# Kernel tuning notes

Hardware: AMD Instinct MI355X
Metric: run time of the kernel (lower is better)

The kernel has to match this reference:

```python
import jax, jax.numpy as jnp
import numpy as np

D_MODEL = 1024
D_STATE = 128
HEAD_DIM = 64
EXPAND = 2
K = 4  # conv_kernel
N_GROUPS = 1
D_INNER = EXPAND * D_MODEL            # 2048
N_HEADS = D_INNER // HEAD_DIM         # 32
D_PROJ = 2 * D_INNER + 2 * N_GROUPS * D_STATE + N_HEADS  # 4384
EPS = 1e-6


def _rmsnorm(x, w):
    return x * jax.lax.rsqrt(jnp.mean(x * x, axis=-1, keepdims=True) + EPS) * w


def setup_inputs() -> dict:
    key = jax.random.key(0)
    ks = jax.random.split(key, 8)
    B, L = 2, 2048
    x = jax.random.normal(ks[0], (B, L, D_MODEL), jnp.float32)
    norm_w = jnp.ones((D_MODEL,), jnp.float32)
    in_proj_w = jax.random.normal(ks[1], (D_PROJ, D_MODEL), jnp.float32) / np.sqrt(D_MODEL).astype(np.float32)
    conv_w = jax.random.normal(ks[2], (D_INNER, K), jnp.float32) / np.sqrt(K).astype(np.float32)
    conv_b = jnp.zeros((D_INNER,), jnp.float32)
    A_log = jnp.log(jax.random.uniform(ks[3], (N_HEADS,), jnp.float32) * 15.0 + 1.0)
    D = jnp.ones((N_HEADS,), jnp.float32)
    dt_bias = jnp.log(jax.random.uniform(ks[4], (N_HEADS,), jnp.float32) * 0.099 + 0.001)
    out_proj_w = jax.random.normal(ks[5], (D_MODEL, D_INNER), jnp.float32) / np.sqrt(D_INNER).astype(np.float32)
    return dict(x=x, norm_w=norm_w, in_proj_w=in_proj_w, conv_w=conv_w, conv_b=conv_b,
                A_log=A_log, D=D, dt_bias=dt_bias, out_proj_w=out_proj_w)


def reference(x, norm_w, in_proj_w, conv_w, conv_b, A_log, D, dt_bias, out_proj_w):
    batch, L, _ = x.shape
    residual = x
    xn = _rmsnorm(x, norm_w)
    proj = jnp.einsum('bld,pd->blp', xn, in_proj_w)  # (B,L,D_PROJ)

    # split fused projection -> z, x_ssm, B, C, dt_raw
    i = 0
    z = proj[:, :, i:i + D_INNER]; i += D_INNER
    x_ssm = proj[:, :, i:i + D_INNER]; i += D_INNER
    bc = N_GROUPS * D_STATE
    Bm = proj[:, :, i:i + bc].reshape(batch, L, N_GROUPS, D_STATE); i += bc
    Cm = proj[:, :, i:i + bc].reshape(batch, L, N_GROUPS, D_STATE); i += bc
    dt_raw = proj[:, :, i:i + N_HEADS]

    # causal depthwise conv1d (left-pad K-1) + SiLU
    xp = jnp.pad(x_ssm, ((0, 0), (K - 1, 0), (0, 0)))
    x_conv = conv_b
    for k in range(K):
        x_conv = x_conv + xp[:, k:k + L, :] * conv_w[:, k]
    x_conv = jax.nn.silu(x_conv)

    xh = x_conv.reshape(batch, L, N_HEADS, HEAD_DIM)
    dt = jax.nn.softplus(dt_raw + dt_bias)          # (B,L,H)
    dA = jnp.exp(-jnp.exp(A_log) * dt)              # (B,L,H)
    dtx = dt[..., None] * xh                        # (B,L,H,P)

    gidx = jnp.arange(N_HEADS) // (N_HEADS // N_GROUPS)
    Bg = Bm[:, :, gidx, :]                          # (B,L,H,N)
    Cg = Cm[:, :, gidx, :]                          # (B,L,H,N)

    def step(h, inp):
        dA_t, dtx_t, B_t, C_t = inp                 # (B,H), (B,H,P), (B,H,N), (B,H,N)
        h = h * dA_t[:, :, None, None] + dtx_t[..., None] * B_t[:, :, None, :]
        y_t = jnp.einsum('bhpn,bhn->bhp', h, C_t)
        return h, y_t

    h0 = jnp.zeros((batch, N_HEADS, HEAD_DIM, D_STATE), jnp.float32)
    xs = (jnp.swapaxes(dA, 0, 1), jnp.swapaxes(dtx, 0, 1),
          jnp.swapaxes(Bg, 0, 1), jnp.swapaxes(Cg, 0, 1))
    _, ys = jax.lax.scan(step, h0, xs)              # ys: (L,B,H,P)
    y = jnp.swapaxes(ys, 0, 1) + D[None, None, :, None] * xh

    y = y.reshape(batch, L, D_INNER) * jax.nn.silu(z)
    return residual + jnp.einsum('bli,di->bld', y, out_proj_w)
```

## Files before the change

kernel.cpp:

```cpp
#include <hip/hip_runtime.h>
#include <hip/hip_bf16.h>

#define L_SEQ 2048
#define DM 1024
#define DI 2048
#define DS 128
#define NH 32
#define HD 64
#define DPROJ 4384
#define DPAD 4480
#define NBATCH 2
#define NCH 8
#define CH 256
#define B_OFF 4096
#define C_OFF 4224
#define DT_OFF 4352
#define SWZ(row) ((((row) ^ ((row) >> 3)) & 7) << 4)

typedef unsigned short u16;
typedef __attribute__((ext_vector_type(8))) short short8;
typedef __attribute__((ext_vector_type(4))) float f32x4;

#define GLL16(g, l)                                                     \
  __builtin_amdgcn_global_load_lds(                                     \
      (const __attribute__((address_space(1))) unsigned int*)(g),       \
      (__attribute__((address_space(3))) unsigned int*)(l), 16, 0, 0)
#define SBAR __builtin_amdgcn_s_barrier()
#define MEMFENCE asm volatile("" ::: "memory")

__device__ __forceinline__ u16 f2bf(float f) {
  union { float f; unsigned u; } c; c.f = f;
  unsigned u = c.u;
  u += 0x7fffu + ((u >> 16) & 1u);
  return (u16)(u >> 16);
}
__device__ __forceinline__ float bf2f(u16 u) {
  return __uint_as_float((unsigned)u << 16);
}
__device__ __forceinline__ float siluf(float x) {
  return x / (1.0f + expf(-x));
}
__device__ __forceinline__ void store_out(u16* C, size_t o, float v) { C[o] = f2bf(v); }
__device__ __forceinline__ void store_out(float* C, size_t o, float v) { C[o] = v; }

__global__ __launch_bounds__(256) void rmsnorm_kernel(
    const float* __restrict__ x, const float* __restrict__ w,
    u16* __restrict__ xnb) {
  int m = blockIdx.x;
  int t = threadIdx.x;
  const float* row = x + (size_t)m * DM;
  float4 v = *(const float4*)(row + t * 4);
  float ss = v.x * v.x + v.y * v.y + v.z * v.z + v.w * v.w;
#pragma unroll
  for (int o = 32; o > 0; o >>= 1) ss += __shfl_xor(ss, o);
  __shared__ float sred[4];
  if ((t & 63) == 0) sred[t >> 6] = ss;
  __syncthreads();
  ss = sred[0] + sred[1] + sred[2] + sred[3];
  float rs = rsqrtf(ss * (1.0f / DM) + 1e-6f);
  float4 wv = *(const float4*)(w + t * 4);
  ushort4 o;
  o.x = f2bf(v.x * rs * wv.x);
  o.y = f2bf(v.y * rs * wv.y);
  o.z = f2bf(v.z * rs * wv.z);
  o.w = f2bf(v.w * rs * wv.w);
  *(ushort4*)(xnb + (size_t)m * DM + t * 4) = o;
}

__global__ __launch_bounds__(256) void cvt_w1_kernel(
    const float* __restrict__ w, u16* __restrict__ o) {
  int r = blockIdx.x;
  int c = threadIdx.x * 4;
  ushort4 u;
  if (r < DPROJ) {
    float4 v = *(const float4*)(w + (size_t)r * DM + c);
    u.x = f2bf(v.x); u.y = f2bf(v.y); u.z = f2bf(v.z); u.w = f2bf(v.w);
  } else {
    u.x = 0; u.y = 0; u.z = 0; u.w = 0;
  }
  *(ushort4*)(o + (size_t)r * DM + c) = u;
}

__global__ __launch_bounds__(256) void cvt_w2_kernel(
    const float* __restrict__ w, u16* __restrict__ o) {
  size_t i = ((size_t)blockIdx.x * 256 + threadIdx.x) * 8;
  float4 v0 = *(const float4*)(w + i);
  float4 v1 = *(const float4*)(w + i + 4);
  ushort4 a, b;
  a.x = f2bf(v0.x); a.y = f2bf(v0.y); a.z = f2bf(v0.z); a.w = f2bf(v0.w);
  b.x = f2bf(v1.x); b.y = f2bf(v1.y); b.z = f2bf(v1.z); b.w = f2bf(v1.w);
  *(ushort4*)(o + i) = a;
  *(ushort4*)(o + i + 4) = b;
}

template <typename OT, bool RES, bool DTS, int BN>
__global__ __launch_bounds__(256, 4) void gemm_bt(
    const u16* __restrict__ A, const u16* __restrict__ Bw,
    OT* __restrict__ C, const float* __restrict__ resid,
    float* __restrict__ dts, int M, int N, int K, int nbx) {
  constexpr int WN = BN / 2;
  constexpr int NJ = WN / 16;
  __shared__ u16 lA[3][128 * 32];
  __shared__ u16 lB[3][BN * 32];
  const int tid = threadIdx.x;
  const int wv = tid >> 6, lane = tid & 63;
  const int wm = wv >> 1, wn = wv & 1;

  const int nwg = gridDim.x;
  const int cpx = nwg >> 3;
  const int wg = blockIdx.x;
  const int swz = (wg & 7) * cpx + (wg >> 3);
  const int m0 = (swz / nbx) * 128, n0 = (swz % nbx) * BN;

  const int rowS = tid >> 2;
  const int colS = (tid & 3) * 8;
  const u16* gA0 = A + (size_t)(m0 + rowS) * K + colS;
  const u16* gA1 = A + (size_t)(m0 + rowS + 64) * K + colS;
  const u16* gB0 = Bw + (size_t)(n0 + rowS) * K + colS;
  const u16* gB1 = Bw + (size_t)(n0 + rowS + 64) * K + colS;

  auto stage = [&](int kt, int buf) {
    const int ko = kt << 5;
    GLL16(gA0 + ko, &lA[buf][wv * 512]);
    GLL16(gA1 + ko, &lA[buf][2048 + wv * 512]);
    GLL16(gB0 + ko, &lB[buf][wv * 512]);
    if (BN == 128) GLL16(gB1 + ko, &lB[buf][2048 + wv * 512]);
  };

  f32x4 acc[4][NJ] = {};
  const int r = lane & 15;
  const int koff = (lane >> 4) * 8;

  auto compute = [&](int buf) {
    short8 af[4], bfr[NJ];
#pragma unroll
    for (int i = 0; i < 4; ++i)
      af[i] = *(const short8*)&lA[buf][(wm * 64 + i * 16 + r) * 32 + koff];
#pragma unroll
    for (int j = 0; j < NJ; ++j)
      bfr[j] = *(const short8*)&lB[buf][(wn * WN + j * 16 + r) * 32 + koff];
#pragma unroll
    for (int i = 0; i < 4; ++i)
#pragma unroll
      for (int j = 0; j < NJ; ++j)
        acc[i][j] = __builtin_amdgcn_mfma_f32_16x16x32_bf16(
            af[i], bfr[j], acc[i][j], 0, 0, 0);
  };

  const int nk = K >> 5;
  stage(0, 0);
  stage(1, 1);
  int cur = 0;
  for (int kt = 0; kt < nk; ++kt) {
    if (kt + 1 < nk) {
      if (BN == 128) asm volatile("s_waitcnt vmcnt(4)" ::: "memory");
      else           asm volatile("s_waitcnt vmcnt(3)" ::: "memory");
    } else {
      asm volatile("s_waitcnt vmcnt(0)" ::: "memory");
    }
    SBAR;
    MEMFENCE;
    if (kt + 2 < nk) {
      int nb = cur + 2; if (nb >= 3) nb -= 3;
      stage(kt + 2, nb);
    }
    compute(cur);
    ++cur; if (cur == 3) cur = 0;
  }

  const int rbase = m0 + wm * 64 + (lane >> 4) * 4;
  const int cbase = n0 + wn * WN + (lane & 15);
#pragma unroll
  for (int i = 0; i < 4; ++i) {
#pragma unroll
    for (int j = 0; j < NJ; ++j) {
      int row0 = rbase + i * 16;
      int col = cbase + j * 16;
#pragma unroll
      for (int rr = 0; rr < 4; ++rr) {
        size_t o = (size_t)(row0 + rr) * N + col;
        float v = acc[i][j][rr];
        if (RES) v += resid[o];
        store_out(C, o, v);
        if (DTS) {
          if (col >= DT_OFF && col < DT_OFF + NH)
            dts[(size_t)(row0 + rr) * NH + (col - DT_OFF)] = v;
        }
      }
    }
  }
}

__global__ __launch_bounds__(256) void conv_kernel(
    const u16* __restrict__ proj, const float* __restrict__ cw,
    const float* __restrict__ cb, u16* __restrict__ xh) {
  int m = blockIdx.x;
  int l = m & (L_SEQ - 1);
  int c0 = threadIdx.x * 8;
  float4 wv[8];
#pragma unroll
  for (int j = 0; j < 8; ++j) wv[j] = *(const float4*)(cw + (size_t)(c0 + j) * 4);
  float acc[8];
#pragma unroll
  for (int j = 0; j < 8; ++j) acc[j] = cb[c0 + j];
#pragma unroll
  for (int k = 0; k < 4; ++k) {
    int lk = l + k - 3;
    if (lk >= 0) {
      short8 rv8 = *(const short8*)(proj + (size_t)(m + k - 3) * DPAD + DI + c0);
#pragma unroll
      for (int j = 0; j < 8; ++j) {
        float wk = (k == 0) ? wv[j].x : (k == 1) ? wv[j].y : (k == 2) ? wv[j].z : wv[j].w;
        acc[j] = fmaf(bf2f((u16)rv8[j]), wk, acc[j]);
      }
    }
  }
  short8 o;
#pragma unroll
  for (int j = 0; j < 8; ++j) o[j] = (short)f2bf(siluf(acc[j]));
  *(short8*)(xh + (size_t)m * DI + c0) = o;
}

__global__ __launch_bounds__(256) void dtda_kernel(
    const float* __restrict__ dts, const float* __restrict__ dt_bias,
    const float* __restrict__ A_log, float* __restrict__ dAdt) {
  int idx = blockIdx.x * 256 + threadIdx.x;
  int h = idx & 31;
  float raw = dts[idx] + dt_bias[h];
  float dt = fmaxf(raw, 0.0f) + log1pf(expf(-fabsf(raw)));
  float a = -expf(A_log[h]) * dt;
  float2 o; o.x = a; o.y = dt;
  *(float2*)(dAdt + (size_t)idx * 2) = o;
}


__global__ __launch_bounds__(512) void scan_state_mfma(
    const u16* __restrict__ proj, const float* __restrict__ dAdt,
    const u16* __restrict__ xhy, float* __restrict__ S,
    float* __restrict__ P) {
  __shared__ u16 sBT[128 * 64];
  __shared__ u16 sXT[64 * 64];
  __shared__ u16 sXW[64 * 64];
  __shared__ float sDt[64], sCum[64], sWs[64], sLam[64];

  const int bid = blockIdx.x;
  const int ch = bid & 7, hh = (bid >> 3) & 31, b = bid >> 8;
  const int tid = threadIdx.x;
  const int w = tid >> 6, l = tid & 63;
  const int tw = w >> 1, half = w & 1;
  const int klane = (l >> 4) * 16;
  const size_t mchunk = (size_t)(b * L_SEQ + ch * CH);

  f32x4 hAcc[4] = {};
  float ctot = 0.0f;

  auto STAGE = [&](int sc) {
    const size_t m0 = mchunk + (size_t)sc * 64;
    {
      const int tp = tid >> 4;
      const int n0 = (tid & 15) * 8;
      const u16* r0 = proj + (m0 + 2 * tp) * DPAD + B_OFF + n0;
      short8 lo8 = *(const short8*)r0;
      short8 hi8 = *(const short8*)(r0 + DPAD);
#pragma unroll
      for (int q = 0; q < 8; ++q) {
        int n = n0 + q;
        unsigned v = (unsigned)(u16)lo8[q] | ((unsigned)(u16)hi8[q] << 16);
        *(unsigned*)((char*)sBT + ((n * 128 + 4 * tp) ^ SWZ(n))) = v;
      }
    }
    {
      const int sx = tid >> 3;
      const int p0 = (tid & 7) * 8;
      short8 xv8 = *(const short8*)(xhy + (m0 + sx) * DI + hh * 64 + p0);
#pragma unroll
      for (int i = 0; i < 8; ++i) {
        int p = p0 + i;
        *(u16*)((char*)sXT + ((p * 128 + 2 * sx) ^ SWZ(p))) = (u16)xv8[i];
      }
    }
    if (tid < 64) {
      float2 ad = *(const float2*)(dAdt + (m0 + tid) * 64 + hh * 2);
      float a = ad.x, dtv = ad.y;
      sDt[tid] = dtv;
      float val = a;
#pragma unroll
      for (int o = 1; o < 64; o <<= 1) {
        float t2 = __shfl_up(val, o);
        if (tid >= o) val += t2;
      }
      sCum[tid] = val;
      float c63 = __shfl(val, 63);
      sWs[tid] = __expf(c63 - val) * dtv;
      sLam[tid] = __expf(val);
    }
  };

  STAGE(0);
  __syncthreads();

  for (int sc = 0; sc < 4; ++sc) {
    {
      int p = tid >> 3, sg = tid & 7;
      int byteX = (p * 128 + sg * 16) ^ SWZ(p);
      short8 xv = *(short8*)((char*)sXT + byteX);
      short8 outp;
#pragma unroll
      for (int j = 0; j < 8; ++j)
        outp[j] = (short)f2bf(bf2f((u16)xv[j]) * sWs[sg * 8 + j]);
      *(short8*)((char*)sXW + byteX) = outp;
    }
    __syncthreads();

    {
      float lam63 = sLam[63];
      ctot += sCum[63];
#pragma unroll
      for (int j = 0; j < 4; ++j) {
        hAcc[j][0] *= lam63; hAcc[j][1] *= lam63;
        hAcc[j][2] *= lam63; hAcc[j][3] *= lam63;
      }
      int prow = tw * 16 + (l & 15);
      short8 aXW[2];
#pragma unroll
      for (int kk = 0; kk < 2; ++kk)
        aXW[kk] = *(short8*)((char*)sXW + ((prow * 128 + kk * 64 + klane) ^ SWZ(prow)));
#pragma unroll
      for (int j = 0; j < 4; ++j) {
        int nrow = (half * 4 + j) * 16 + (l & 15);
#pragma unroll
        for (int kk = 0; kk < 2; ++kk) {
          short8 bBT = *(short8*)((char*)sBT + ((nrow * 128 + kk * 64 + klane) ^ SWZ(nrow)));
          hAcc[j] = __builtin_amdgcn_mfma_f32_16x16x32_bf16(aXW[kk], bBT, hAcc[j], 0, 0, 0);
        }
      }
    }
    __syncthreads();
    if (sc < 3) STAGE(sc + 1);
    __syncthreads();
  }

  float* Sb = S + (size_t)((b * 32 + hh) * NCH + ch) * 8192;
  const int p0 = tw * 16 + (l >> 4) * 4;
#pragma unroll
  for (int j = 0; j < 4; ++j) {
    int n = (half * 4 + j) * 16 + (l & 15);
#pragma unroll
    for (int r = 0; r < 4; ++r)
      Sb[(p0 + r) * 128 + n] = hAcc[j][r];
  }
  if (tid == 0) P[(b * 32 + hh) * NCH + ch] = __expf(ctot);
}

__global__ __launch_bounds__(256) void combine_kernel(
    float* __restrict__ S, const float* __restrict__ P) {
  int tid = blockIdx.x * 256 + threadIdx.x;
  int bh = tid >> 13, pn = tid & 8191;
  size_t base = (size_t)bh * NCH * 8192 + pn;
  float E = 0.0f;
#pragma unroll
  for (int c = 0; c < NCH; ++c) {
    size_t o = base + (size_t)c * 8192;
    float Sc = S[o];
    S[o] = E;
    E = fmaf(P[bh * NCH + c], E, Sc);
  }
}

__global__ __launch_bounds__(512) void scan_y_mfma(
    const u16* __restrict__ proj, const float* __restrict__ dAdt,
    const u16* __restrict__ xhy, const float* __restrict__ Dv,
    const float* __restrict__ S, u16* __restrict__ yb) {
  __shared__ u16 sC[64 * 128];
  __shared__ u16 sB[64 * 128];
  __shared__ u16 sHb[64 * 128];
  __shared__ u16 sBT[128 * 64];
  __shared__ u16 sXT[64 * 64];
  __shared__ u16 sXW[64 * 64];
  __shared__ u16 sW[64 * 64];
  __shared__ float sDt[64], sCum[64], sWs[64], sLam[64];

  const int bid = blockIdx.x;
  const int ch = bid & 7, hh = (bid >> 3) & 31, b = bid >> 8;
  const int tid = threadIdx.x;
  const int w = tid >> 6, l = tid & 63;
  const int tw = w >> 1, half = w & 1;
  const int klane = (l >> 4) * 16;
  const float Dh = Dv[hh];
  const size_t mchunk = (size_t)(b * L_SEQ + ch * CH);

  f32x4 hAcc[4];
  {
    const float* Sb = S + (size_t)((b * 32 + hh) * NCH + ch) * 8192;
    const int p0 = tw * 16 + (l >> 4) * 4;
#pragma unroll
    for (int j = 0; j < 4; ++j) {
      int n = (half * 4 + j) * 16 + (l & 15);
#pragma unroll
      for (int r = 0; r < 4; ++r)
        hAcc[j][r] = Sb[(p0 + r) * 128 + n];
    }
    int p = tid >> 3, sg = tid & 7;
#pragma unroll
    for (int i = 0; i < 4; ++i) {
      float4 v = *(const float4*)(Sb + p * 128 + sg * 16 + 4 * i);
      ushort4 u;
      u.x = f2bf(v.x); u.y = f2bf(v.y); u.z = f2bf(v.z); u.w = f2bf(v.w);
      *(ushort4*)((char*)sHb + ((p * 256 + (sg * 16 + 4 * i) * 2) ^ SWZ(p))) = u;
    }
  }

  auto STAGE = [&](int sc) {
    const size_t m0 = mchunk + (size_t)sc * 64;
    {
      const int tp = tid >> 4;
      const int n0 = (tid & 15) * 8;
      const u16* r0 = proj + (m0 + 2 * tp) * DPAD;
      short8 b0 = *(const short8*)(r0 + B_OFF + n0);
      short8 b1 = *(const short8*)(r0 + DPAD + B_OFF + n0);
      short8 c0v = *(const short8*)(r0 + C_OFF + n0);
      short8 c1v = *(const short8*)(r0 + DPAD + C_OFF + n0);
      *(short8*)((char*)sB + ((2 * tp * 256 + n0 * 2) ^ SWZ(2 * tp))) = b0;
      *(short8*)((char*)sB + (((2 * tp + 1) * 256 + n0 * 2) ^ SWZ(2 * tp + 1))) = b1;
      *(short8*)((char*)sC + ((2 * tp * 256 + n0 * 2) ^ SWZ(2 * tp))) = c0v;
      *(short8*)((char*)sC + (((2 * tp + 1) * 256 + n0 * 2) ^ SWZ(2 * tp + 1))) = c1v;
#pragma unroll
      for (int q = 0; q < 8; ++q) {
        int n = n0 + q;
        unsigned v = (unsigned)(u16)b0[q] | ((unsigned)(u16)b1[q] << 16);
        *(unsigned*)((char*)sBT + ((n * 128 + 4 * tp) ^ SWZ(n))) = v;
      }
    }
    {
      const int sx = tid >> 3;
      const int p0 = (tid & 7) * 8;
      short8 xv8 = *(const short8*)(xhy + (m0 + sx) * DI + hh * 64 + p0);
#pragma unroll
      for (int i = 0; i < 8; ++i) {
        int p = p0 + i;
        *(u16*)((char*)sXT + ((p * 128 + 2 * sx) ^ SWZ(p))) = (u16)xv8[i];
      }
    }
    if (tid < 64) {
      float2 ad = *(const float2*)(dAdt + (m0 + tid) * 64 + hh * 2);
      float a = ad.x, dtv = ad.y;
      sDt[tid] = dtv;
      float val = a;
#pragma unroll
      for (int o = 1; o < 64; o <<= 1) {
        float t2 = __shfl_up(val, o);
        if (tid >= o) val += t2;
      }
      sCum[tid] = val;
      float c63 = __shfl(val, 63);
      sWs[tid] = __expf(c63 - val) * dtv;
      sLam[tid] = __expf(val);
    }
  };

  STAGE(0);
  __syncthreads();

  for (int sc = 0; sc < 4; ++sc) {
    const size_t m0 = mchunk + (size_t)sc * 64;
    {
      int p = tid >> 3, sg = tid & 7;
      int byteX = (p * 128 + sg * 16) ^ SWZ(p);
      short8 xv = *(short8*)((char*)sXT + byteX);
      short8 outp;
#pragma unroll
      for (int j = 0; j < 8; ++j)
        outp[j] = (short)f2bf(bf2f((u16)xv[j]) * sWs[sg * 8 + j]);
      *(short8*)((char*)sXW + byteX) = outp;
    }
    __syncthreads();

    const int trow = tw * 16 + (l & 15);
    short8 aC[4];
#pragma unroll
    for (int kk = 0; kk < 4; ++kk)
      aC[kk] = *(short8*)((char*)sC + ((trow * 256 + kk * 64 + klane) ^ SWZ(trow)));

    {
      f32x4 g[2] = {};
#pragma unroll
      for (int sv2 = 0; sv2 < 2; ++sv2) {
        int srow = (half * 2 + sv2) * 16 + (l & 15);
#pragma unroll
        for (int kk = 0; kk < 4; ++kk) {
          short8 bB = *(short8*)((char*)sB + ((srow * 256 + kk * 64 + klane) ^ SWZ(srow)));
          g[sv2] = __builtin_amdgcn_mfma_f32_16x16x32_bf16(aC[kk], bB, g[sv2], 0, 0, 0);
        }
      }
#pragma unroll
      for (int sv2 = 0; sv2 < 2; ++sv2) {
        int s = (half * 2 + sv2) * 16 + (l & 15);
        float dts_ = sDt[s], cums = sCum[s];
#pragma unroll
        for (int r = 0; r < 4; ++r) {
          int t = tw * 16 + (l >> 4) * 4 + r;
          float v = (t >= s) ? g[sv2][r] * __expf(sCum[t] - cums) * dts_ : 0.0f;
          *(u16*)((char*)sW + ((t * 128 + 2 * s) ^ SWZ(t))) = f2bf(v);
        }
      }
    }
    __syncthreads();

    f32x4 y1[2] = {}, y2[2] = {};
    float lamv[4], lam63 = sLam[63];
#pragma unroll
    for (int r = 0; r < 4; ++r) lamv[r] = sLam[tw * 16 + (l >> 4) * 4 + r];
    {
      short8 aW[2];
#pragma unroll
      for (int kk = 0; kk < 2; ++kk)
        aW[kk] = *(short8*)((char*)sW + ((trow * 128 + kk * 64 + klane) ^ SWZ(trow)));
#pragma unroll
      for (int pv2 = 0; pv2 < 2; ++pv2) {
        int prow = (half * 2 + pv2) * 16 + (l & 15);
#pragma unroll
        for (int kk = 0; kk < 2; ++kk) {
          short8 bX = *(short8*)((char*)sXT + ((prow * 128 + kk * 64 + klane) ^ SWZ(prow)));
          y1[pv2] = __builtin_amdgcn_mfma_f32_16x16x32_bf16(aW[kk], bX, y1[pv2], 0, 0, 0);
        }
#pragma unroll
        for (int kk = 0; kk < 4; ++kk) {
          short8 bH = *(short8*)((char*)sHb + ((prow * 256 + kk * 64 + klane) ^ SWZ(prow)));
          y2[pv2] = __builtin_amdgcn_mfma_f32_16x16x32_bf16(aC[kk], bH, y2[pv2], 0, 0, 0);
        }
      }
#pragma unroll
      for (int j = 0; j < 4; ++j) {
        hAcc[j][0] *= lam63; hAcc[j][1] *= lam63;
        hAcc[j][2] *= lam63; hAcc[j][3] *= lam63;
      }
      short8 aXW[2];
#pragma unroll
      for (int kk = 0; kk < 2; ++kk)
        aXW[kk] = *(short8*)((char*)sXW + ((trow * 128 + kk * 64 + klane) ^ SWZ(trow)));
#pragma unroll
      for (int j = 0; j < 4; ++j) {
        int nrow = (half * 4 + j) * 16 + (l & 15);
#pragma unroll
        for (int kk = 0; kk < 2; ++kk) {
          short8 bBT = *(short8*)((char*)sBT + ((nrow * 128 + kk * 64 + klane) ^ SWZ(nrow)));
          hAcc[j] = __builtin_amdgcn_mfma_f32_16x16x32_bf16(aXW[kk], bBT, hAcc[j], 0, 0, 0);
        }
      }
    }
    __syncthreads();

    {
#pragma unroll
      for (int j = 0; j < 4; ++j) {
        int n = (half * 4 + j) * 16 + (l & 15);
#pragma unroll
        for (int r = 0; r < 4; ++r) {
          int p = tw * 16 + (l >> 4) * 4 + r;
          *(u16*)((char*)sHb + ((p * 256 + 2 * n) ^ SWZ(p))) = f2bf(hAcc[j][r]);
        }
      }
#pragma unroll
      for (int pv2 = 0; pv2 < 2; ++pv2) {
        int p = (half * 2 + pv2) * 16 + (l & 15);
#pragma unroll
        for (int r = 0; r < 4; ++r) {
          int t = tw * 16 + (l >> 4) * 4 + r;
          int col = hh * 64 + p;
          size_t gy = (m0 + t) * DI + col;
          float xv = bf2f(xhy[gy]);
          float yv = y1[pv2][r] + lamv[r] * y2[pv2][r] + Dh * xv;
          float zv = bf2f(proj[(m0 + t) * DPAD + col]);
          yb[gy] = f2bf(yv * siluf(zv));
        }
      }
      if (sc < 3) STAGE(sc + 1);
    }
    __syncthreads();
  }
}

extern "C" void kernel_launch(void* const* d_in, const int* in_sizes, int n_in,
                              void* d_out, int out_size, void* d_ws, size_t ws_size,
                              hipStream_t stream) {
  const float* x      = (const float*)d_in[0];
  const float* norm_w = (const float*)d_in[1];
  const float* w1     = (const float*)d_in[2];
  const float* cw     = (const float*)d_in[3];
  const float* cb     = (const float*)d_in[4];
  const float* A_log  = (const float*)d_in[5];
  const float* Dv     = (const float*)d_in[6];
  const float* dt_b   = (const float*)d_in[7];
  const float* w2     = (const float*)d_in[8];
  float* out = (float*)d_out;

  char* ws = (char*)d_ws;
  u16*   xnb  = (u16*)(ws);
  u16*   w1b  = (u16*)(ws + 8388608);
  u16*   w2b  = (u16*)(ws + 17563648);
  u16*   proj = (u16*)(ws + 21757952);
  float* dts  = (float*)(ws + 58458112);
  u16*   xhy  = (u16*)(ws + 58982400);
  float* dAdt = (float*)(ws + 75759616);
  u16*   yb   = (u16*)(ws + 76808192);
  float* S    = (float*)(ws + 93585408);
  float* P    = (float*)(ws + 110362624);

  const int M = NBATCH * L_SEQ;

  rmsnorm_kernel<<<M, 256, 0, stream>>>(x, norm_w, xnb);
  cvt_w1_kernel<<<DPAD, 256, 0, stream>>>(w1, w1b);
  cvt_w2_kernel<<<1024, 256, 0, stream>>>(w2, w2b);
  gemm_bt<u16, false, true, 128><<<(DPAD / 128) * (M / 128), 256, 0, stream>>>(
      xnb, w1b, proj, nullptr, dts, M, DPAD, DM, DPAD / 128);
  conv_kernel<<<M, 256, 0, stream>>>(proj, cw, cb, xhy);
  dtda_kernel<<<M * NH / 256, 256, 0, stream>>>(dts, dt_b, A_log, dAdt);
  scan_state_mfma<<<512, 512, 0, stream>>>(proj, dAdt, xhy, S, P);
  combine_kernel<<<2048, 256, 0, stream>>>(S, P);
  scan_y_mfma<<<512, 512, 0, stream>>>(proj, dAdt, xhy, Dv, S, yb);
  gemm_bt<float, true, false, 64><<<(DM / 64) * (M / 128), 256, 0, stream>>>(
      yb, w2b, out, x, nullptr, M, DM, DI, DM / 64);
}
```

Before: 209.9 us.

## Use 256x256-tile double-buffered MFMA GEMM for the input projection

```diff
diff --git a/kernel.cpp b/kernel.cpp
--- a/kernel.cpp
+++ b/kernel.cpp
@@ -8,7 +8,7 @@
 #define NH 32
 #define HD 64
 #define DPROJ 4384
-#define DPAD 4480
+#define DPAD 4608
 #define NBATCH 2
 #define NCH 8
 #define CH 256
@@ -93,11 +93,128 @@
   *(ushort4*)(o + i + 4) = b;
 }
 
-template <typename OT, bool RES, bool DTS, int BN>
+__global__ __launch_bounds__(512, 2) void gemm256(
+    const u16* __restrict__ A, const u16* __restrict__ Bw,
+    u16* __restrict__ C, float* __restrict__ dts,
+    int M, int N, int K, int nbx) {
+  __shared__ u16 lA[2][256 * 64];
+  __shared__ u16 lB[2][256 * 64];
+  const int tid = threadIdx.x;
+  const int w = tid >> 6, lane = tid & 63;
+  const int wm = w >> 2, wn = w & 3;
+
+  const int nwg = gridDim.x, cpx = nwg >> 3, wg = blockIdx.x;
+  const int swz = (wg & 7) * cpx + (wg >> 3);
+  const int m0 = (swz / nbx) * 256, n0 = (swz % nbx) * 256;
+
+  const int rowS = tid >> 3;
+  const int colS = ((tid & 7) * 8) ^ ((tid & 32) ? 16 : 0);
+  const u16* gA = A + (size_t)(m0 + rowS) * K + colS;
+  const u16* gB = Bw + (size_t)(n0 + rowS) * K + colS;
+
+  auto stageBh = [&](int kt, int buf, int h) {
+    const int ko = kt * 64;
+#pragma unroll
+    for (int q = 0; q < 2; ++q)
+      GLL16(gB + (size_t)(h * 128 + q * 64) * K + ko,
+            &lB[buf][h * 8192 + q * 4096 + w * 512]);
+  };
+  auto stageAq = [&](int kt, int buf, int q) {
+    const int ko = kt * 64;
+#pragma unroll
+    for (int h = 0; h < 2; ++h)
+      GLL16(gA + (size_t)(h * 128 + q * 64) * K + ko,
+            &lA[buf][h * 8192 + q * 4096 + w * 512]);
+  };
+
+  f32x4 acc[8][4] = {};
+  short8 bfr[4][2];
+  const int kswz = ((lane >> 4) * 16) ^ ((lane & 4) ? 32 : 0);
+  const int arow = wm * 128 + (lane & 15);
+  const int brow = wn * 64 + (lane & 15);
+
+  const int NT = K >> 6;
+  stageBh(0, 0, 0); stageBh(0, 0, 1); stageAq(0, 0, 0); stageAq(0, 0, 1);
+  asm volatile("s_waitcnt vmcnt(0)" ::: "memory");
+  SBAR;
+  MEMFENCE;
+
+  for (int kt = 0; kt < NT; ++kt) {
+    const int b = kt & 1;
+    const bool more = (kt + 1 < NT);
+#pragma unroll
+    for (int p = 0; p < 4; ++p) {
+      if (p == 0) {
+#pragma unroll
+        for (int j = 0; j < 4; ++j)
+#pragma unroll
+          for (int ks = 0; ks < 2; ++ks)
+            bfr[j][ks] = *(const short8*)((const char*)&lB[b][0] +
+                ((brow + j * 16) << 7) + ks * 64 + kswz);
+      }
+      short8 af[2][2];
+#pragma unroll
+      for (int ii = 0; ii < 2; ++ii)
+#pragma unroll
+        for (int ks = 0; ks < 2; ++ks)
+          af[ii][ks] = *(const short8*)((const char*)&lA[b][0] +
+              ((arow + (2 * p + ii) * 16) << 7) + ks * 64 + kswz);
+      if (more) {
+        if (p == 0) stageBh(kt + 1, b ^ 1, 0);
+        else if (p == 1) stageBh(kt + 1, b ^ 1, 1);
+        else if (p == 2) stageAq(kt + 1, b ^ 1, 0);
+        else stageAq(kt + 1, b ^ 1, 1);
+      }
+      MEMFENCE;
+      SBAR;
+      MEMFENCE;
+      __builtin_amdgcn_s_setprio(1);
+#pragma unroll
+      for (int ii = 0; ii < 2; ++ii)
+#pragma unroll
+        for (int j = 0; j < 4; ++j) {
+          acc[2 * p + ii][j] = __builtin_amdgcn_mfma_f32_16x16x32_bf16(
+              af[ii][0], bfr[j][0], acc[2 * p + ii][j], 0, 0, 0);
+          acc[2 * p + ii][j] = __builtin_amdgcn_mfma_f32_16x16x32_bf16(
+              af[ii][1], bfr[j][1], acc[2 * p + ii][j], 0, 0, 0);
+        }
+      __builtin_amdgcn_s_setprio(0);
+      if (p == 1) {
+        if (more) asm volatile("s_waitcnt vmcnt(4)" ::: "memory");
+        else      asm volatile("s_waitcnt vmcnt(0)" ::: "memory");
+      }
+      if (p == 3) {
+        if (more) asm volatile("s_waitcnt vmcnt(2)" ::: "memory");
+        else      asm volatile("s_waitcnt vmcnt(0)" ::: "memory");
+      }
+      MEMFENCE;
+      SBAR;
+      MEMFENCE;
+    }
+  }
+
+  const int rb = m0 + wm * 128 + (lane >> 4) * 4;
+  const int cb = n0 + wn * 64 + (lane & 15);
+#pragma unroll
+  for (int i = 0; i < 8; ++i)
+#pragma unroll
+    for (int j = 0; j < 4; ++j)
+#pragma unroll
+      for (int rr = 0; rr < 4; ++rr) {
+        int row = rb + i * 16 + rr, col = cb + j * 16;
+        size_t o = (size_t)row * N + col;
+        float v = acc[i][j][rr];
+        C[o] = f2bf(v);
+        if (col >= DT_OFF && col < DT_OFF + NH)
+          dts[(size_t)row * NH + (col - DT_OFF)] = v;
+      }
+}
+
+template <typename OT, bool RES, int BN>
 __global__ __launch_bounds__(256, 4) void gemm_bt(
     const u16* __restrict__ A, const u16* __restrict__ Bw,
     OT* __restrict__ C, const float* __restrict__ resid,
-    float* __restrict__ dts, int M, int N, int K, int nbx) {
+    int M, int N, int K, int nbx) {
   constexpr int WN = BN / 2;
   constexpr int NJ = WN / 16;
   __shared__ u16 lA[3][128 * 32];
@@ -182,10 +299,6 @@
         float v = acc[i][j][rr];
         if (RES) v += resid[o];
         store_out(C, o, v);
-        if (DTS) {
-          if (col >= DT_OFF && col < DT_OFF + NH)
-            dts[(size_t)(row0 + rr) * NH + (col - DT_OFF)] = v;
-        }
       }
     }
   }
@@ -232,7 +345,6 @@
   float2 o; o.x = a; o.y = dt;
   *(float2*)(dAdt + (size_t)idx * 2) = o;
 }
-
 
 __global__ __launch_bounds__(512) void scan_state_mfma(
     const u16* __restrict__ proj, const float* __restrict__ dAdt,
@@ -597,27 +709,27 @@
   char* ws = (char*)d_ws;
   u16*   xnb  = (u16*)(ws);
   u16*   w1b  = (u16*)(ws + 8388608);
-  u16*   w2b  = (u16*)(ws + 17563648);
-  u16*   proj = (u16*)(ws + 21757952);
-  float* dts  = (float*)(ws + 58458112);
-  u16*   xhy  = (u16*)(ws + 58982400);
-  float* dAdt = (float*)(ws + 75759616);
-  u16*   yb   = (u16*)(ws + 76808192);
-  float* S    = (float*)(ws + 93585408);
-  float* P    = (float*)(ws + 110362624);
+  u16*   w2b  = (u16*)(ws + 17825792);
+  u16*   proj = (u16*)(ws + 22020096);
+  float* dts  = (float*)(ws + 59768832);
+  u16*   xhy  = (u16*)(ws + 60293120);
+  float* dAdt = (float*)(ws + 77070336);
+  u16*   yb   = (u16*)(ws + 78118912);
+  float* S    = (float*)(ws + 94896128);
+  float* P    = (float*)(ws + 111673344);
 
   const int M = NBATCH * L_SEQ;
 
   rmsnorm_kernel<<<M, 256, 0, stream>>>(x, norm_w, xnb);
   cvt_w1_kernel<<<DPAD, 256, 0, stream>>>(w1, w1b);
   cvt_w2_kernel<<<1024, 256, 0, stream>>>(w2, w2b);
-  gemm_bt<u16, false, true, 128><<<(DPAD / 128) * (M / 128), 256, 0, stream>>>(
-      xnb, w1b, proj, nullptr, dts, M, DPAD, DM, DPAD / 128);
+  gemm256<<<(DPAD / 256) * (M / 256), 512, 0, stream>>>(
+      xnb, w1b, proj, dts, M, DPAD, DM, DPAD / 256);
   conv_kernel<<<M, 256, 0, stream>>>(proj, cw, cb, xhy);
   dtda_kernel<<<M * NH / 256, 256, 0, stream>>>(dts, dt_b, A_log, dAdt);
   scan_state_mfma<<<512, 512, 0, stream>>>(proj, dAdt, xhy, S, P);
   combine_kernel<<<2048, 256, 0, stream>>>(S, P);
   scan_y_mfma<<<512, 512, 0, stream>>>(proj, dAdt, xhy, Dv, S, yb);
-  gemm_bt<float, true, false, 64><<<(DM / 64) * (M / 128), 256, 0, stream>>>(
-      yb, w2b, out, x, nullptr, M, DM, DI, DM / 64);
-}
+  gemm_bt<float, true, 64><<<(DM / 64) * (M / 128), 256, 0, stream>>>(
+      yb, w2b, out, x, M, DM, DI, DM / 64);
+}
```

New measurement: 222.8 us. 6.2% more time.
